# Performance work log

Measured on AMD Instinct MI355X. Metric: run time of the kernel, lower is better.

Reference implementation:

```python
import jax, jax.numpy as jnp
import numpy as np

N_HEAD = 16
MASKED_BIAS = -10000.0

def setup_inputs() -> dict:
    key = jax.random.key(0)
    k1, k2, k3 = jax.random.split(key, 3)
    B, S, D = 4, 1024, 1024
    return {
        "hidden_states": jax.random.normal(k1, (B, S, D), dtype=jnp.float32),
        "c_attn_w": jax.random.normal(k2, (D, 3 * D), dtype=jnp.float32) * 0.02,
        "c_attn_b": jnp.zeros((3 * D,), dtype=jnp.float32),
        "c_proj_w": jax.random.normal(k3, (D, D), dtype=jnp.float32) * 0.02,
        "c_proj_b": jnp.zeros((D,), dtype=jnp.float32),
    }

def reference(hidden_states, c_attn_w, c_attn_b, c_proj_w, c_proj_b):
    B, S, D = hidden_states.shape
    H = N_HEAD
    hd = D // H
    qkv = hidden_states @ c_attn_w + c_attn_b          # [B,S,3D]
    q, k, v = jnp.split(qkv, 3, axis=-1)
    # split heads -> [B,H,S,hd]
    q = q.reshape(B, S, H, hd).transpose(0, 2, 1, 3)
    k = k.reshape(B, S, H, hd).transpose(0, 2, 1, 3)
    v = v.reshape(B, S, H, hd).transpose(0, 2, 1, 3)
    w = jnp.einsum("bhqd,bhkd->bhqk", q, k) / jnp.sqrt(jnp.float32(hd))
    causal = jnp.tril(jnp.ones((S, S), dtype=bool))
    w = jnp.where(causal, w, jnp.asarray(MASKED_BIAS, w.dtype))
    w = jax.nn.softmax(w, axis=-1)
    a = jnp.einsum("bhqk,bhkd->bhqd", w, v)            # [B,H,S,hd]
    a = a.transpose(0, 2, 1, 3).reshape(B, S, D)       # merge heads
    out = a @ c_proj_w + c_proj_b
    return out
```

## Files before the change

kernel.cpp:

```cpp
#include <hip/hip_runtime.h>
#include <hip/hip_bf16.h>

typedef __attribute__((ext_vector_type(8))) short bf16x8;
typedef __attribute__((ext_vector_type(4))) float f32x4;

#define QSCALE 0.1803368801111244f

static __device__ inline short f2bf(float f) {
    union { float f; unsigned u; } x; x.f = f;
    unsigned r = x.u + 0x7FFF + ((x.u >> 16) & 1);
    return (short)(r >> 16);
}

static __device__ inline void gload_lds16(const void* g, void* l) {
    __builtin_amdgcn_global_load_lds(
        (const __attribute__((address_space(1))) unsigned*)g,
        (__attribute__((address_space(3))) unsigned*)l, 16, 0, 0);
}

__global__ __launch_bounds__(256) void prep(
    const float* __restrict__ hs, const float* __restrict__ w1,
    const float* __restrict__ w2,
    short* __restrict__ Hb, short* __restrict__ W1t, short* __restrict__ W2t)
{
    __shared__ short Ts[64][72];
    const int t = threadIdx.x;
    const int blk = blockIdx.x;

    if (blk < 1024) {
        #pragma unroll
        for (int it = 0; it < 4; ++it) {
            long i4 = (long)blk * 1024 + it * 256 + t;
            float4 v = reinterpret_cast<const float4*>(hs)[i4];
            short4 s4;
            s4.x = f2bf(v.x); s4.y = f2bf(v.y); s4.z = f2bf(v.z); s4.w = f2bf(v.w);
            reinterpret_cast<short4*>(Hb)[i4] = s4;
        }
        return;
    }

    const float* W; short* Wt; int NC, tx, ty;
    if (blk < 1792) { int id = blk - 1024; W = w1; Wt = W1t; NC = 3072; tx = id % 48; ty = id / 48; }
    else            { int id = blk - 1792; W = w2; Wt = W2t; NC = 1024; tx = id % 16; ty = id / 16; }
    const int r0 = ty * 64;
    const int c0 = tx * 64;

    #pragma unroll
    for (int it = 0; it < 4; ++it) {
        int slot = t + it * 256;
        int row = slot >> 4, c4 = (slot & 15) << 2;
        float4 v = *reinterpret_cast<const float4*>(&W[(long)(r0 + row) * NC + c0 + c4]);
        Ts[c4 + 0][row] = f2bf(v.x);
        Ts[c4 + 1][row] = f2bf(v.y);
        Ts[c4 + 2][row] = f2bf(v.z);
        Ts[c4 + 3][row] = f2bf(v.w);
    }
    __syncthreads();
    #pragma unroll
    for (int it = 0; it < 2; ++it) {
        int slot = t + it * 256;
        int orow = slot >> 3, ok8 = (slot & 7) << 3;
        *reinterpret_cast<bf16x8*>(&Wt[(long)(c0 + orow) * 1024 + r0 + ok8]) =
            *reinterpret_cast<const bf16x8*>(&Ts[orow][ok8]);
    }
}

__global__ __launch_bounds__(256) void qkv_gemm(
    const short* __restrict__ A,
    const short* __restrict__ Bt,
    const float* __restrict__ bias,
    short* __restrict__ Qw, short* __restrict__ Kw)
{
    __shared__ short As[128 * 64];
    __shared__ short Bs[128 * 64];

    const int t  = threadIdx.x;
    const int w  = t >> 6, l = t & 63;
    const int g  = l >> 4, lr = l & 15;
    const int m0 = blockIdx.x * 128;
    const int n0 = blockIdx.y * 128;
    const int wm = (w >> 1) * 64, wn = (w & 1) * 64;
    const int srow = l >> 3, sc = (l & 7) << 3;

    f32x4 acc[4][4] = {};

    for (int k0 = 0; k0 < 1024; k0 += 64) {
        #pragma unroll
        for (int it = 0; it < 4; ++it) {
            const int seg = w * 4 + it;
            const int row = seg * 8 + srow;
            gload_lds16(&A [(long)(m0 + row) * 1024 + k0 + sc], &As[seg * 512]);
            gload_lds16(&Bt[(long)(n0 + row) * 1024 + k0 + sc], &Bs[seg * 512]);
        }
        __syncthreads();
        #pragma unroll
        for (int kk = 0; kk < 64; kk += 32) {
            bf16x8 af[4], bfv[4];
            #pragma unroll
            for (int mi = 0; mi < 4; ++mi)
                af[mi] = *reinterpret_cast<const bf16x8*>(&As[(wm + mi * 16 + lr) * 64 + kk + g * 8]);
            #pragma unroll
            for (int ni = 0; ni < 4; ++ni)
                bfv[ni] = *reinterpret_cast<const bf16x8*>(&Bs[(wn + ni * 16 + lr) * 64 + kk + g * 8]);
            #pragma unroll
            for (int mi = 0; mi < 4; ++mi)
                #pragma unroll
                for (int ni = 0; ni < 4; ++ni)
                    acc[mi][ni] = __builtin_amdgcn_mfma_f32_16x16x32_bf16(
                        af[mi], bfv[ni], acc[mi][ni], 0, 0, 0);
        }
        __syncthreads();
    }

    #pragma unroll
    for (int mi = 0; mi < 4; ++mi) {
        #pragma unroll
        for (int ni = 0; ni < 4; ++ni) {
            int n = n0 + wn + ni * 16 + lr;
            float bv = bias[n];
            int sel = n >> 10, d = n & 1023;
            int h = d >> 6, hi = d & 63;
            short* dst = sel ? Kw : Qw;
            float sc_ = sel ? 1.0f : QSCALE;
            #pragma unroll
            for (int r = 0; r < 4; ++r) {
                int m = m0 + wm + mi * 16 + g * 4 + r;
                int b = m >> 10, s = m & 1023;
                dst[(((b * 16 + h) * 1024 + s) * 64 + hi)] = f2bf((acc[mi][ni][r] + bv) * sc_);
            }
        }
    }
}

__global__ __launch_bounds__(256) void vT_gemm(
    const short* __restrict__ A,
    const short* __restrict__ Bt,
    const float* __restrict__ bias,
    short* __restrict__ Vt)
{
    __shared__ short As[128 * 64];
    __shared__ short Bs[128 * 64];

    const int t  = threadIdx.x;
    const int w  = t >> 6, l = t & 63;
    const int g  = l >> 4, lr = l & 15;
    const int m0 = blockIdx.x * 128;
    const int n0 = blockIdx.y * 128;
    const int wm = (w >> 1) * 64, wn = (w & 1) * 64;
    const int srow = l >> 3, sc = (l & 7) << 3;

    f32x4 acc[4][4] = {};

    for (int k0 = 0; k0 < 1024; k0 += 64) {
        #pragma unroll
        for (int it = 0; it < 4; ++it) {
            const int seg = w * 4 + it;
            const int row = seg * 8 + srow;
            gload_lds16(&A [(long)(m0 + row) * 1024 + k0 + sc], &As[seg * 512]);
            gload_lds16(&Bt[(long)(n0 + row) * 1024 + k0 + sc], &Bs[seg * 512]);
        }
        __syncthreads();
        #pragma unroll
        for (int kk = 0; kk < 64; kk += 32) {
            bf16x8 af[4], bfv[4];
            #pragma unroll
            for (int mi = 0; mi < 4; ++mi)
                af[mi] = *reinterpret_cast<const bf16x8*>(&As[(wm + mi * 16 + lr) * 64 + kk + g * 8]);
            #pragma unroll
            for (int ni = 0; ni < 4; ++ni)
                bfv[ni] = *reinterpret_cast<const bf16x8*>(&Bs[(wn + ni * 16 + lr) * 64 + kk + g * 8]);
            #pragma unroll
            for (int mi = 0; mi < 4; ++mi)
                #pragma unroll
                for (int ni = 0; ni < 4; ++ni)
                    acc[mi][ni] = __builtin_amdgcn_mfma_f32_16x16x32_bf16(
                        af[mi], bfv[ni], acc[mi][ni], 0, 0, 0);
        }
        __syncthreads();
    }

    #pragma unroll
    for (int mi = 0; mi < 4; ++mi)
        #pragma unroll
        for (int r = 0; r < 4; ++r) {
            int m = m0 + wm + mi * 16 + g * 4 + r;
            float bv = bias[2048 + m];
            #pragma unroll
            for (int ni = 0; ni < 4; ++ni) {
                int n = n0 + wn + ni * 16 + lr;
                int b = n >> 10, s = n & 1023;
                Vt[(long)b * 1048576 + (long)m * 1024 + s] = f2bf(acc[mi][ni][r] + bv);
            }
        }
}

__global__ __launch_bounds__(256) void attn(
    const short* __restrict__ Qw, const short* __restrict__ Kw,
    const short* __restrict__ Vt, short* __restrict__ Aw)
{
    __shared__ short Kb[2][4096];
    __shared__ short Vb[2][4096];
    __shared__ short Ps[4][16 * 72];

    const int t = threadIdx.x;
    const int w = t >> 6, l = t & 63, g = l >> 4, lr = l & 15;
    const int blk = blockIdx.x;
    const int qt = 15 - (blk >> 6);
    const int bh = blk & 63;
    const int b = bh >> 4, h = bh & 15;
    const short* Qg = Qw + ((long)bh << 16);
    const short* Kg = Kw + ((long)bh << 16);
    const short* Vg = Vt + ((long)bh << 16);

    bf16x8 qf[2];
    {
        const short* qr = Qg + (long)(qt * 64 + w * 16 + lr) * 64;
        qf[0] = *(const bf16x8*)(qr + g * 8);
        qf[1] = *(const bf16x8*)(qr + 32 + g * 8);
    }

    float rsum[4] = {0.f, 0.f, 0.f, 0.f};
    f32x4 o[4] = {};
    short* ps = &Ps[w][0];

    auto stage = [&](int d, int kt) {
        #pragma unroll
        for (int it = 0; it < 2; ++it) {
            int seg = (w << 1) + it;
            int row = (seg << 3) + (l >> 3);
            int slot = (l & 7) ^ (row & 7);
            gload_lds16(Kg + ((long)((kt << 6) + row) << 6) + (slot << 3), &Kb[d][seg << 9]);
            gload_lds16(Vg + ((long)row << 10) + (kt << 6) + (slot << 3), &Vb[d][seg << 9]);
        }
    };

    stage(0, 0);
    __syncthreads();

    for (int kt = 0; kt <= qt; ++kt) {
        const int cur = kt & 1;
        if (kt < qt) stage(cur ^ 1, kt + 1);
        const bool diag = (kt == qt);

        f32x4 s[4] = {};
        #pragma unroll
        for (int kk = 0; kk < 2; ++kk)
            #pragma unroll
            for (int nt = 0; nt < 4; ++nt) {
                bf16x8 kf = *(const bf16x8*)&Kb[cur][((nt * 16 + lr) << 6) +
                            ((((kk << 2) + g) ^ (lr & 7)) << 3)];
                s[nt] = __builtin_amdgcn_mfma_f32_16x16x32_bf16(qf[kk], kf, s[nt], 0, 0, 0);
            }
        if (diag) {
            #pragma unroll
            for (int nt = 0; nt < 4; ++nt)
                #pragma unroll
                for (int r = 0; r < 4; ++r)
                    if (nt * 16 + lr > w * 16 + g * 4 + r) s[nt][r] = -1e30f;
        }

        #pragma unroll
        for (int nt = 0; nt < 4; ++nt)
            #pragma unroll
            for (int r = 0; r < 4; ++r) {
                float p = exp2f(s[nt][r]);
                rsum[r] += p;
                ps[(g * 4 + r) * 72 + nt * 16 + lr] = f2bf(p);
            }

        asm volatile("s_waitcnt lgkmcnt(0)" ::: "memory");

        #pragma unroll
        for (int kk = 0; kk < 2; ++kk) {
            bf16x8 pf = *(const bf16x8*)&ps[lr * 72 + kk * 32 + g * 8];
            #pragma unroll
            for (int nt = 0; nt < 4; ++nt) {
                bf16x8 vf = *(const bf16x8*)&Vb[cur][((nt * 16 + lr) << 6) +
                            ((((kk << 2) + g) ^ (lr & 7)) << 3)];
                o[nt] = __builtin_amdgcn_mfma_f32_16x16x32_bf16(pf, vf, o[nt], 0, 0, 0);
            }
        }
        __syncthreads();
    }

    float rinv[4];
    #pragma unroll
    for (int r = 0; r < 4; ++r) {
        float rs = rsum[r];
        rs += __shfl_xor(rs, 1, 64);
        rs += __shfl_xor(rs, 2, 64);
        rs += __shfl_xor(rs, 4, 64);
        rs += __shfl_xor(rs, 8, 64);
        rinv[r] = 1.0f / rs;
    }
    #pragma unroll
    for (int nt = 0; nt < 4; ++nt)
        #pragma unroll
        for (int r = 0; r < 4; ++r) {
            float val = o[nt][r] * rinv[r];
            int srow = qt * 64 + w * 16 + g * 4 + r;
            Aw[((long)(b * 1024 + srow) << 10) + h * 64 + nt * 16 + lr] = f2bf(val);
        }
}

__global__ __launch_bounds__(256) void proj_gemm(
    const short* __restrict__ A,
    const short* __restrict__ Bt,
    const float* __restrict__ bias,
    float* __restrict__ out)
{
    __shared__ short As[128 * 64];
    __shared__ short Bs[128 * 64];

    const int t  = threadIdx.x;
    const int w  = t >> 6, l = t & 63;
    const int g  = l >> 4, lr = l & 15;
    const int m0 = blockIdx.x * 128;
    const int n0 = blockIdx.y * 128;
    const int wm = (w >> 1) * 64, wn = (w & 1) * 64;
    const int srow = l >> 3, sc = (l & 7) << 3;

    f32x4 acc[4][4] = {};

    for (int k0 = 0; k0 < 1024; k0 += 64) {
        #pragma unroll
        for (int it = 0; it < 4; ++it) {
            const int seg = w * 4 + it;
            const int row = seg * 8 + srow;
            gload_lds16(&A [(long)(m0 + row) * 1024 + k0 + sc], &As[seg * 512]);
            gload_lds16(&Bt[(long)(n0 + row) * 1024 + k0 + sc], &Bs[seg * 512]);
        }
        __syncthreads();
        #pragma unroll
        for (int kk = 0; kk < 64; kk += 32) {
            bf16x8 af[4], bfv[4];
            #pragma unroll
            for (int mi = 0; mi < 4; ++mi)
                af[mi] = *reinterpret_cast<const bf16x8*>(&As[(wm + mi * 16 + lr) * 64 + kk + g * 8]);
            #pragma unroll
            for (int ni = 0; ni < 4; ++ni)
                bfv[ni] = *reinterpret_cast<const bf16x8*>(&Bs[(wn + ni * 16 + lr) * 64 + kk + g * 8]);
            #pragma unroll
            for (int mi = 0; mi < 4; ++mi)
                #pragma unroll
                for (int ni = 0; ni < 4; ++ni)
                    acc[mi][ni] = __builtin_amdgcn_mfma_f32_16x16x32_bf16(
                        af[mi], bfv[ni], acc[mi][ni], 0, 0, 0);
        }
        __syncthreads();
    }

    #pragma unroll
    for (int mi = 0; mi < 4; ++mi)
        #pragma unroll
        for (int ni = 0; ni < 4; ++ni) {
            int n = n0 + wn + ni * 16 + lr;
            float bv = bias[n];
            #pragma unroll
            for (int r = 0; r < 4; ++r) {
                int m = m0 + wm + mi * 16 + g * 4 + r;
                out[m * 1024 + n] = acc[mi][ni][r] + bv;
            }
        }
}

extern "C" void kernel_launch(void* const* d_in, const int* in_sizes, int n_in,
                              void* d_out, int out_size, void* d_ws, size_t ws_size,
                              hipStream_t stream)
{
    const float* hs     = (const float*)d_in[0];
    const float* attn_w = (const float*)d_in[1];
    const float* attn_b = (const float*)d_in[2];
    const float* proj_w = (const float*)d_in[3];
    const float* proj_b = (const float*)d_in[4];
    float* out = (float*)d_out;

    short* Hb  = (short*)d_ws;
    short* W1t = Hb  + 4194304L;
    short* W2t = W1t + 3145728L;
    short* Qw  = W2t + 1048576L;
    short* Kw  = Qw  + 4194304L;
    short* Vt  = Kw  + 4194304L;
    short* Aw  = Hb;

    prep<<<2048, 256, 0, stream>>>(hs, attn_w, proj_w, Hb, W1t, W2t);
    qkv_gemm<<<dim3(32, 16), 256, 0, stream>>>(Hb, W1t, attn_b, Qw, Kw);
    vT_gemm<<<dim3(8, 32), 256, 0, stream>>>(W1t + 2097152L, Hb, attn_b, Vt);
    attn<<<1024, 256, 0, stream>>>(Qw, Kw, Vt, Aw);
    proj_gemm<<<dim3(32, 8), 256, 0, stream>>>(Aw, W2t, proj_b, out);
}
```

Before: 115.2 us.

## Merge QK and V GEMMs into one launch, swizzle blocks, prioritize MFMA in attention

Combines the QK GEMM and the transposed-V GEMM into a single 768-block kernel that picks its role and tile from a swizzled block index. This removes one launch and the tail of the smaller grid. The proj GEMM gets a similar 1D swizzled block mapping, meant to spread co-running blocks across the XCDs for cache locality. In the attention kernel, s_setprio raises wave priority around the MFMA sections, so matrix work from one wave can interleave with softmax work from others. The merged kernel carries a divergent epilogue branch, and changing the block order may alter L2 reuse patterns.

Result: slower. 118.3 us (+2.7%).

```diff
diff --git a/kernel.cpp b/kernel.cpp
--- a/kernel.cpp
+++ b/kernel.cpp
@@ -65,11 +65,11 @@
     }
 }
 
-__global__ __launch_bounds__(256) void qkv_gemm(
-    const short* __restrict__ A,
-    const short* __restrict__ Bt,
+__global__ __launch_bounds__(256) void qkv_all(
+    const short* __restrict__ Hb,
+    const short* __restrict__ W1t,
     const float* __restrict__ bias,
-    short* __restrict__ Qw, short* __restrict__ Kw)
+    short* __restrict__ Qw, short* __restrict__ Kw, short* __restrict__ Vt)
 {
     __shared__ short As[128 * 64];
     __shared__ short Bs[128 * 64];
@@ -77,10 +77,23 @@
     const int t  = threadIdx.x;
     const int w  = t >> 6, l = t & 63;
     const int g  = l >> 4, lr = l & 15;
-    const int m0 = blockIdx.x * 128;
-    const int n0 = blockIdx.y * 128;
     const int wm = (w >> 1) * 64, wn = (w & 1) * 64;
     const int srow = l >> 3, sc = (l & 7) << 3;
+
+    const int swz = (blockIdx.x & 7) * 96 + (blockIdx.x >> 3);
+    const bool isQK = (swz < 512);
+    const short *Ap, *Btp;
+    int m0, n0;
+    if (isQK) {
+        m0 = (swz & 31) * 128;
+        n0 = (swz >> 5) * 128;
+        Ap = Hb; Btp = W1t;
+    } else {
+        int id = swz - 512;
+        m0 = (id & 7) * 128;
+        n0 = (id >> 3) * 128;
+        Ap = W1t + 2097152L; Btp = Hb;
+    }
 
     f32x4 acc[4][4] = {};
 
@@ -89,8 +102,8 @@
         for (int it = 0; it < 4; ++it) {
             const int seg = w * 4 + it;
             const int row = seg * 8 + srow;
-            gload_lds16(&A [(long)(m0 + row) * 1024 + k0 + sc], &As[seg * 512]);
-            gload_lds16(&Bt[(long)(n0 + row) * 1024 + k0 + sc], &Bs[seg * 512]);
+            gload_lds16(&Ap [(long)(m0 + row) * 1024 + k0 + sc], &As[seg * 512]);
+            gload_lds16(&Btp[(long)(n0 + row) * 1024 + k0 + sc], &Bs[seg * 512]);
         }
         __syncthreads();
         #pragma unroll
@@ -112,86 +125,40 @@
         __syncthreads();
     }
 
-    #pragma unroll
-    for (int mi = 0; mi < 4; ++mi) {
-        #pragma unroll
-        for (int ni = 0; ni < 4; ++ni) {
-            int n = n0 + wn + ni * 16 + lr;
-            float bv = bias[n];
-            int sel = n >> 10, d = n & 1023;
-            int h = d >> 6, hi = d & 63;
-            short* dst = sel ? Kw : Qw;
-            float sc_ = sel ? 1.0f : QSCALE;
+    if (isQK) {
+        #pragma unroll
+        for (int mi = 0; mi < 4; ++mi) {
+            #pragma unroll
+            for (int ni = 0; ni < 4; ++ni) {
+                int n = n0 + wn + ni * 16 + lr;
+                float bv = bias[n];
+                int sel = n >> 10, d = n & 1023;
+                int h = d >> 6, hi = d & 63;
+                short* dst = sel ? Kw : Qw;
+                float sc_ = sel ? 1.0f : QSCALE;
+                #pragma unroll
+                for (int r = 0; r < 4; ++r) {
+                    int m = m0 + wm + mi * 16 + g * 4 + r;
+                    int b = m >> 10, s = m & 1023;
+                    dst[(((b * 16 + h) * 1024 + s) * 64 + hi)] = f2bf((acc[mi][ni][r] + bv) * sc_);
+                }
+            }
+        }
+    } else {
+        #pragma unroll
+        for (int mi = 0; mi < 4; ++mi)
             #pragma unroll
             for (int r = 0; r < 4; ++r) {
                 int m = m0 + wm + mi * 16 + g * 4 + r;
-                int b = m >> 10, s = m & 1023;
-                dst[(((b * 16 + h) * 1024 + s) * 64 + hi)] = f2bf((acc[mi][ni][r] + bv) * sc_);
-            }
-        }
-    }
-}
-
-__global__ __launch_bounds__(256) void vT_gemm(
-    const short* __restrict__ A,
-    const short* __restrict__ Bt,
-    const float* __restrict__ bias,
-    short* __restrict__ Vt)
-{
-    __shared__ short As[128 * 64];
-    __shared__ short Bs[128 * 64];
-
-    const int t  = threadIdx.x;
-    const int w  = t >> 6, l = t & 63;
-    const int g  = l >> 4, lr = l & 15;
-    const int m0 = blockIdx.x * 128;
-    const int n0 = blockIdx.y * 128;
-    const int wm = (w >> 1) * 64, wn = (w & 1) * 64;
-    const int srow = l >> 3, sc = (l & 7) << 3;
-
-    f32x4 acc[4][4] = {};
-
-    for (int k0 = 0; k0 < 1024; k0 += 64) {
-        #pragma unroll
-        for (int it = 0; it < 4; ++it) {
-            const int seg = w * 4 + it;
-            const int row = seg * 8 + srow;
-            gload_lds16(&A [(long)(m0 + row) * 1024 + k0 + sc], &As[seg * 512]);
-            gload_lds16(&Bt[(long)(n0 + row) * 1024 + k0 + sc], &Bs[seg * 512]);
-        }
-        __syncthreads();
-        #pragma unroll
-        for (int kk = 0; kk < 64; kk += 32) {
-            bf16x8 af[4], bfv[4];
-            #pragma unroll
-            for (int mi = 0; mi < 4; ++mi)
-                af[mi] = *reinterpret_cast<const bf16x8*>(&As[(wm + mi * 16 + lr) * 64 + kk + g * 8]);
-            #pragma unroll
-            for (int ni = 0; ni < 4; ++ni)
-                bfv[ni] = *reinterpret_cast<const bf16x8*>(&Bs[(wn + ni * 16 + lr) * 64 + kk + g * 8]);
-            #pragma unroll
-            for (int mi = 0; mi < 4; ++mi)
-                #pragma unroll
-                for (int ni = 0; ni < 4; ++ni)
-                    acc[mi][ni] = __builtin_amdgcn_mfma_f32_16x16x32_bf16(
-                        af[mi], bfv[ni], acc[mi][ni], 0, 0, 0);
-        }
-        __syncthreads();
-    }
-
-    #pragma unroll
-    for (int mi = 0; mi < 4; ++mi)
-        #pragma unroll
-        for (int r = 0; r < 4; ++r) {
-            int m = m0 + wm + mi * 16 + g * 4 + r;
-            float bv = bias[2048 + m];
-            #pragma unroll
-            for (int ni = 0; ni < 4; ++ni) {
-                int n = n0 + wn + ni * 16 + lr;
-                int b = n >> 10, s = n & 1023;
-                Vt[(long)b * 1048576 + (long)m * 1024 + s] = f2bf(acc[mi][ni][r] + bv);
-            }
-        }
+                float bv = bias[2048 + m];
+                #pragma unroll
+                for (int ni = 0; ni < 4; ++ni) {
+                    int n = n0 + wn + ni * 16 + lr;
+                    int b = n >> 10, s = n & 1023;
+                    Vt[(long)b * 1048576 + (long)m * 1024 + s] = f2bf(acc[mi][ni][r] + bv);
+                }
+            }
+    }
 }
 
 __global__ __launch_bounds__(256) void attn(
@@ -243,6 +210,7 @@
         const bool diag = (kt == qt);
 
         f32x4 s[4] = {};
+        __builtin_amdgcn_s_setprio(1);
         #pragma unroll
         for (int kk = 0; kk < 2; ++kk)
             #pragma unroll
@@ -251,6 +219,7 @@
                             ((((kk << 2) + g) ^ (lr & 7)) << 3)];
                 s[nt] = __builtin_amdgcn_mfma_f32_16x16x32_bf16(qf[kk], kf, s[nt], 0, 0, 0);
             }
+        __builtin_amdgcn_s_setprio(0);
         if (diag) {
             #pragma unroll
             for (int nt = 0; nt < 4; ++nt)
@@ -270,6 +239,7 @@
 
         asm volatile("s_waitcnt lgkmcnt(0)" ::: "memory");
 
+        __builtin_amdgcn_s_setprio(1);
         #pragma unroll
         for (int kk = 0; kk < 2; ++kk) {
             bf16x8 pf = *(const bf16x8*)&ps[lr * 72 + kk * 32 + g * 8];
@@ -280,6 +250,7 @@
                 o[nt] = __builtin_amdgcn_mfma_f32_16x16x32_bf16(pf, vf, o[nt], 0, 0, 0);
             }
         }
+        __builtin_amdgcn_s_setprio(0);
         __syncthreads();
     }
 
@@ -315,8 +286,9 @@
     const int t  = threadIdx.x;
     const int w  = t >> 6, l = t & 63;
     const int g  = l >> 4, lr = l & 15;
-    const int m0 = blockIdx.x * 128;
-    const int n0 = blockIdx.y * 128;
+    const int swz = (blockIdx.x & 7) * 32 + (blockIdx.x >> 3);
+    const int m0 = (swz & 31) * 128;
+    const int n0 = (swz >> 5) * 128;
     const int wm = (w >> 1) * 64, wn = (w & 1) * 64;
     const int srow = l >> 3, sc = (l & 7) << 3;
 
@@ -384,8 +356,7 @@
     short* Aw  = Hb;
 
     prep<<<2048, 256, 0, stream>>>(hs, attn_w, proj_w, Hb, W1t, W2t);
-    qkv_gemm<<<dim3(32, 16), 256, 0, stream>>>(Hb, W1t, attn_b, Qw, Kw);
-    vT_gemm<<<dim3(8, 32), 256, 0, stream>>>(W1t + 2097152L, Hb, attn_b, Vt);
+    qkv_all<<<768, 256, 0, stream>>>(Hb, W1t, attn_b, Qw, Kw, Vt);
     attn<<<1024, 256, 0, stream>>>(Qw, Kw, Vt, Aw);
-    proj_gemm<<<dim3(32, 8), 256, 0, stream>>>(Aw, W2t, proj_b, out);
-}
+    proj_gemm<<<256, 256, 0, stream>>>(Aw, W2t, proj_b, out);
+}
```
